# Kernel tuning notes

Measured on AMD Instinct MI355X. Metric: run time of the kernel, lower is better.

## Reference

```python
import jax, jax.numpy as jnp
import numpy as np

E = 8            # num_experts
DIM = 2880       # model dim
HID = 2880       # expert hidden dim (mlp1 outputs 2*HID, interleaved glu/linear)
T = 16384        # total dispatched tokens, evenly split across experts
SWIGLU_LIMIT = 7.0
ALPHA = 1.702


def swiglu(x, alpha=ALPHA, limit=SWIGLU_LIMIT):
    # interleaved: even channels -> glu gate, odd channels -> linear
    x_glu = x[..., ::2]
    x_lin = x[..., 1::2]
    x_glu = jnp.minimum(x_glu, limit)
    x_lin = jnp.clip(x_lin, -limit, limit)
    return x_glu * jax.nn.sigmoid(alpha * x_glu) * (x_lin + 1.0)


def setup_inputs() -> dict:
    key = jax.random.key(0)
    k1, k2, k3, k4, k5 = jax.random.split(key, 5)
    scale = 0.02
    x = jax.random.normal(k1, (T, DIM), dtype=jnp.float32)
    num_tokens_per_expert = jnp.full((E,), T // E, dtype=jnp.int64)
    mlp1_weight = jax.random.normal(k2, (E, 2 * HID, DIM), dtype=jnp.float32) * scale
    mlp1_bias = jax.random.normal(k3, (E, 2 * HID), dtype=jnp.float32) * scale
    mlp2_weight = jax.random.normal(k4, (E, DIM, HID), dtype=jnp.float32) * scale
    mlp2_bias = jax.random.normal(k5, (E, DIM), dtype=jnp.float32) * scale
    return {
        "x": x,
        "num_tokens_per_expert": num_tokens_per_expert,
        "mlp1_weight": mlp1_weight,
        "mlp1_bias": mlp1_bias,
        "mlp2_weight": mlp2_weight,
        "mlp2_bias": mlp2_bias,
    }


def reference(x, num_tokens_per_expert, mlp1_weight, mlp1_bias, mlp2_weight, mlp2_bias):
    # Equal token counts per expert (as constructed): grouped GEMM == batched GEMM
    # over a reshaped [E, T/E, DIM] view. tp_degree == 1 so ScaleBiasForward is identity.
    tpe = T // E
    xg = x.reshape(E, tpe, DIM)                                  # [E, t, D]
    h = jnp.einsum("etd,ehd->eth", xg, mlp1_weight)              # [E, t, 2H]
    h = h + mlp1_bias[:, None, :]
    h = swiglu(h)                                                # [E, t, H]
    out = jnp.einsum("eth,edh->etd", h, mlp2_weight)             # [E, t, D]
    out = out + mlp2_bias[:, None, :]
    return out.reshape(T, DIM)
```

## Files before the change

### kernel.cpp

```cpp
#include <hip/hip_runtime.h>
#include <hip/hip_bf16.h>


#define TT   16384
#define DIM_ 2880
#define HID_ 2880
#define NE   8
#define TPE  2048
#define KDIM 2880

typedef __attribute__((ext_vector_type(8))) short short8;
typedef __attribute__((ext_vector_type(4))) float f32x4;

__device__ __forceinline__ unsigned short f2bf(float f) {
  unsigned u = __builtin_bit_cast(unsigned, f);
  u += 0x7fffu + ((u >> 16) & 1u);
  return (unsigned short)(u >> 16);
}

__global__ void __launch_bounds__(256) cvt_f32_bf16(const float* __restrict__ src,
                                                    unsigned short* __restrict__ dst,
                                                    long n) {
  long i = ((long)blockIdx.x * 256 + threadIdx.x) * 8;
  if (i >= n) return;
  float4 a = *(const float4*)(src + i);
  float4 b = *(const float4*)(src + i + 4);
  union { unsigned short u[8]; short8 v; } r;
  r.u[0] = f2bf(a.x); r.u[1] = f2bf(a.y); r.u[2] = f2bf(a.z); r.u[3] = f2bf(a.w);
  r.u[4] = f2bf(b.x); r.u[5] = f2bf(b.y); r.u[6] = f2bf(b.z); r.u[7] = f2bf(b.w);
  *(short8*)(dst + i) = r.v;
}

template<int BN, int FN, bool FUSE_SWIGLU>
__global__ void __launch_bounds__(256) gemm_bt(const unsigned short* __restrict__ A,
                                               const unsigned short* __restrict__ B,
                                               const float* __restrict__ bias,
                                               void* __restrict__ Cout,
                                               int M, int N) {
  constexpr int BM = 128, BK = 64;
  const int tid  = threadIdx.x;
  const int lane = tid & 63;
  const int wid  = tid >> 6;
  const int wr   = wid >> 1, wc = wid & 1;
  const int e    = blockIdx.z;
  const int m0   = blockIdx.y * BM;
  const int n0   = blockIdx.x * BN;

  __shared__ unsigned short As[BM * BK];
  __shared__ unsigned short Bs[BN * BK];

  const unsigned short* Ae = A + (size_t)e * M * KDIM + (size_t)m0 * KDIM;
  const unsigned short* Be = B + (size_t)e * N * KDIM + (size_t)n0 * KDIM;

  f32x4 acc[4][FN] = {};

  const int srow = tid >> 3;
  const int scol = (tid & 7) * 8;

  for (int kt = 0; kt < KDIM / BK; ++kt) {
    const unsigned short* ak = Ae + kt * BK + scol;
    const unsigned short* bk = Be + kt * BK + scol;
#pragma unroll
    for (int j = 0; j < BM / 32; ++j)
      __builtin_amdgcn_global_load_lds(
          (const __attribute__((address_space(1))) unsigned int*)(ak + (size_t)(j * 32 + srow) * KDIM),
          (__attribute__((address_space(3))) unsigned int*)(&As[j * 2048 + tid * 8]),
          16, 0, 0);
#pragma unroll
    for (int j = 0; j < BN / 32; ++j)
      __builtin_amdgcn_global_load_lds(
          (const __attribute__((address_space(1))) unsigned int*)(bk + (size_t)(j * 32 + srow) * KDIM),
          (__attribute__((address_space(3))) unsigned int*)(&Bs[j * 2048 + tid * 8]),
          16, 0, 0);
    __syncthreads();

#pragma unroll
    for (int ks = 0; ks < 2; ++ks) {
      short8 af[4];
#pragma unroll
      for (int fm = 0; fm < 4; ++fm)
        af[fm] = *(const short8*)&As[(wr * 64 + fm * 16 + (lane & 15)) * BK + ks * 32 + (lane >> 4) * 8];
#pragma unroll
      for (int fn = 0; fn < FN; ++fn) {
        short8 bf = *(const short8*)&Bs[(wc * (FN * 16) + fn * 16 + (lane & 15)) * BK + ks * 32 + (lane >> 4) * 8];
#pragma unroll
        for (int fm = 0; fm < 4; ++fm)
          acc[fm][fn] = __builtin_amdgcn_mfma_f32_16x16x32_bf16(af[fm], bf, acc[fm][fn], 0, 0, 0);
      }
    }
    __syncthreads();
  }

  const float* be = bias + (size_t)e * N;
  if constexpr (FUSE_SWIGLU) {
    unsigned short* ha = (unsigned short*)Cout + (size_t)e * M * (N / 2);
#pragma unroll
    for (int fm = 0; fm < 4; ++fm)
#pragma unroll
      for (int fn = 0; fn < FN; ++fn) {
        const int col = n0 + wc * (FN * 16) + fn * 16 + (lane & 15);
        const float bc = be[col];
#pragma unroll
        for (int j = 0; j < 4; ++j) {
          const int row = m0 + wr * 64 + fm * 16 + (lane >> 4) * 4 + j;
          float v = acc[fm][fn][j] + bc;
          float p = __shfl_xor(v, 1);
          if (!(lane & 1)) {
            float g  = fminf(v, 7.0f);
            float l2 = fminf(fmaxf(p, -7.0f), 7.0f);
            float act = g / (1.0f + __expf(-1.702f * g)) * (l2 + 1.0f);
            ha[(size_t)row * (N / 2) + (col >> 1)] = f2bf(act);
          }
        }
      }
  } else {
    float* out = (float*)Cout + (size_t)e * M * N;
#pragma unroll
    for (int fm = 0; fm < 4; ++fm)
#pragma unroll
      for (int fn = 0; fn < FN; ++fn) {
        const int col = n0 + wc * (FN * 16) + fn * 16 + (lane & 15);
        const float bc = be[col];
#pragma unroll
        for (int j = 0; j < 4; ++j) {
          const int row = m0 + wr * 64 + fm * 16 + (lane >> 4) * 4 + j;
          out[(size_t)row * N + col] = acc[fm][fn][j] + bc;
        }
      }
  }
}

extern "C" void kernel_launch(void* const* d_in, const int* in_sizes, int n_in,
                              void* d_out, int out_size, void* d_ws, size_t ws_size,
                              hipStream_t stream) {
  const float* x  = (const float*)d_in[0];
  const float* w1 = (const float*)d_in[2];
  const float* b1 = (const float*)d_in[3];
  const float* w2 = (const float*)d_in[4];
  const float* b2 = (const float*)d_in[5];

  unsigned short* xb  = (unsigned short*)d_ws;
  unsigned short* w1b = xb  + (size_t)TT * DIM_;
  unsigned short* w2b = w1b + (size_t)NE * 2 * HID_ * DIM_;
  unsigned short* ha  = w2b + (size_t)NE * DIM_ * HID_;

  const long nx = (long)TT * DIM_;
  const long n1 = (long)NE * 2 * HID_ * DIM_;
  const long n2 = (long)NE * DIM_ * HID_;
  cvt_f32_bf16<<<(int)(nx / 2048), 256, 0, stream>>>(x,  xb,  nx);
  cvt_f32_bf16<<<(int)(n1 / 2048), 256, 0, stream>>>(w1, w1b, n1);
  cvt_f32_bf16<<<(int)(n2 / 2048), 256, 0, stream>>>(w2, w2b, n2);

  dim3 g1(2 * HID_ / 128, TPE / 128, NE);
  gemm_bt<128, 4, true><<<g1, 256, 0, stream>>>(xb, w1b, b1, ha, TPE, 2 * HID_);

  dim3 g2(DIM_ / 96, TPE / 128, NE);
  gemm_bt<96, 3, false><<<g2, 256, 0, stream>>>(ha, w2b, b2, (float*)d_out, TPE, DIM_);
}
```

Measured before the change: 1.388 ms.

## Replace GEMMs with 8-wave 256x192 double-buffered pipelined kernel with LDS swizzle

Replaces the single-buffered 128xBN GEMM with a 512-thread kernel using 256x192 tiles. Global-to-LDS loads are double-buffered with explicit vmcnt waits so the next K tile streams in while MFMAs run. The LDS layout is XOR-swizzled to avoid bank conflicts, and block indices are remapped to group tiles for better L2 reuse. The larger tile raises register pressure and shrinks the grid, which could hurt occupancy or leave a tail wave.

```diff
diff --git a/kernel.cpp b/kernel.cpp
--- a/kernel.cpp
+++ b/kernel.cpp
@@ -8,6 +8,7 @@
 #define NE   8
 #define TPE  2048
 #define KDIM 2880
+#define NT   45
 
 typedef __attribute__((ext_vector_type(8))) short short8;
 typedef __attribute__((ext_vector_type(4))) float f32x4;
@@ -31,99 +32,141 @@
   *(short8*)(dst + i) = r.v;
 }
 
-template<int BN, int FN, bool FUSE_SWIGLU>
-__global__ void __launch_bounds__(256) gemm_bt(const unsigned short* __restrict__ A,
-                                               const unsigned short* __restrict__ B,
-                                               const float* __restrict__ bias,
-                                               void* __restrict__ Cout,
-                                               int M, int N) {
-  constexpr int BM = 128, BK = 64;
+template<bool FUSE_SWIGLU>
+__global__ void __launch_bounds__(512, 2) gemm8(const unsigned short* __restrict__ A,
+                                                const unsigned short* __restrict__ B,
+                                                const float* __restrict__ bias,
+                                                void* __restrict__ Cout,
+                                                int M, int N) {
+  __shared__ unsigned short As[2][256 * 64];
+  __shared__ unsigned short Bs[2][192 * 64];
+
   const int tid  = threadIdx.x;
   const int lane = tid & 63;
   const int wid  = tid >> 6;
-  const int wr   = wid >> 1, wc = wid & 1;
+  const int wr   = wid >> 2;
+  const int wc   = wid & 3;
   const int e    = blockIdx.z;
-  const int m0   = blockIdx.y * BM;
-  const int n0   = blockIdx.x * BN;
-
-  __shared__ unsigned short As[BM * BK];
-  __shared__ unsigned short Bs[BN * BK];
-
-  const unsigned short* Ae = A + (size_t)e * M * KDIM + (size_t)m0 * KDIM;
-  const unsigned short* Be = B + (size_t)e * N * KDIM + (size_t)n0 * KDIM;
-
-  f32x4 acc[4][FN] = {};
+
+  const int ntn   = N / 192;
+  const int ntm   = M / 256;
+  const int per_e = ntn * ntm;
+  const int bid   = blockIdx.x;
+  const int swz   = (bid & 7) * (per_e >> 3) + (bid >> 3);
+  const int m0    = (swz / ntn) * 256;
+  const int n0    = (swz % ntn) * 192;
 
   const int srow = tid >> 3;
-  const int scol = (tid & 7) * 8;
-
-  for (int kt = 0; kt < KDIM / BK; ++kt) {
-    const unsigned short* ak = Ae + kt * BK + scol;
-    const unsigned short* bk = Be + kt * BK + scol;
-#pragma unroll
-    for (int j = 0; j < BM / 32; ++j)
+  const int scol = (((tid & 7) ^ (srow & 7)) << 4) >> 1;
+  const unsigned short* Aexp = A + ((size_t)e * M + m0 + srow) * KDIM + scol;
+  const unsigned short* Bexp = B + ((size_t)e * N + n0 + srow) * KDIM + scol;
+
+  auto stage = [&](int buf, int kt) {
+    const unsigned short* asrc = Aexp + (size_t)kt * 64;
+#pragma unroll
+    for (int j = 0; j < 4; ++j)
       __builtin_amdgcn_global_load_lds(
-          (const __attribute__((address_space(1))) unsigned int*)(ak + (size_t)(j * 32 + srow) * KDIM),
-          (__attribute__((address_space(3))) unsigned int*)(&As[j * 2048 + tid * 8]),
+          (const __attribute__((address_space(1))) unsigned int*)(asrc + (size_t)(j * 64) * KDIM),
+          (__attribute__((address_space(3))) unsigned int*)(&As[buf][j * 4096 + tid * 8]),
           16, 0, 0);
-#pragma unroll
-    for (int j = 0; j < BN / 32; ++j)
+    const unsigned short* bsrc = Bexp + (size_t)kt * 64;
+#pragma unroll
+    for (int j = 0; j < 3; ++j)
       __builtin_amdgcn_global_load_lds(
-          (const __attribute__((address_space(1))) unsigned int*)(bk + (size_t)(j * 32 + srow) * KDIM),
-          (__attribute__((address_space(3))) unsigned int*)(&Bs[j * 2048 + tid * 8]),
+          (const __attribute__((address_space(1))) unsigned int*)(bsrc + (size_t)(j * 64) * KDIM),
+          (__attribute__((address_space(3))) unsigned int*)(&Bs[buf][j * 4096 + tid * 8]),
           16, 0, 0);
-    __syncthreads();
-
-#pragma unroll
-    for (int ks = 0; ks < 2; ++ks) {
-      short8 af[4];
-#pragma unroll
-      for (int fm = 0; fm < 4; ++fm)
-        af[fm] = *(const short8*)&As[(wr * 64 + fm * 16 + (lane & 15)) * BK + ks * 32 + (lane >> 4) * 8];
-#pragma unroll
-      for (int fn = 0; fn < FN; ++fn) {
-        short8 bf = *(const short8*)&Bs[(wc * (FN * 16) + fn * 16 + (lane & 15)) * BK + ks * 32 + (lane >> 4) * 8];
-#pragma unroll
-        for (int fm = 0; fm < 4; ++fm)
-          acc[fm][fn] = __builtin_amdgcn_mfma_f32_16x16x32_bf16(af[fm], bf, acc[fm][fn], 0, 0, 0);
-      }
+  };
+
+  const int arow_off = (wr * 128 + (lane & 15)) * 128;
+  const int brow_off = (wc * 48  + (lane & 15)) * 128;
+  const int swzb = (lane & 7) << 4;
+  const int kb   = ((lane >> 4) & 3) * 16;
+  const int c0 = kb ^ swzb;
+  const int c1 = (64 + kb) ^ swzb;
+
+  f32x4 acc[8][3] = {};
+
+  stage(0, 0);
+  stage(1, 1);
+  asm volatile("s_waitcnt vmcnt(7)" ::: "memory");
+  __builtin_amdgcn_s_barrier();
+
+  for (int t = 0; t < NT; ++t) {
+    const int cur = t & 1;
+    const char* aB = (const char*)(&As[cur][0]) + arow_off;
+    const char* bB = (const char*)(&Bs[cur][0]) + brow_off;
+
+    short8 a0[8], a1[8], b0[3], b1[3];
+#pragma unroll
+    for (int fm = 0; fm < 8; ++fm) {
+      a0[fm] = *(const short8*)(aB + fm * 2048 + c0);
+      a1[fm] = *(const short8*)(aB + fm * 2048 + c1);
     }
-    __syncthreads();
+#pragma unroll
+    for (int fn = 0; fn < 3; ++fn) {
+      b0[fn] = *(const short8*)(bB + fn * 2048 + c0);
+      b1[fn] = *(const short8*)(bB + fn * 2048 + c1);
+    }
+
+#pragma unroll
+    for (int fn = 0; fn < 3; ++fn)
+#pragma unroll
+      for (int fm = 0; fm < 8; ++fm)
+        acc[fm][fn] = __builtin_amdgcn_mfma_f32_16x16x32_bf16(a0[fm], b0[fn], acc[fm][fn], 0, 0, 0);
+
+    asm volatile("s_waitcnt lgkmcnt(0)" ::: "memory");
+    __builtin_amdgcn_s_barrier();
+
+    const bool more = (t + 2 < NT);
+    if (more) stage(cur, t + 2);
+
+    __builtin_amdgcn_s_setprio(1);
+#pragma unroll
+    for (int fn = 0; fn < 3; ++fn)
+#pragma unroll
+      for (int fm = 0; fm < 8; ++fm)
+        acc[fm][fn] = __builtin_amdgcn_mfma_f32_16x16x32_bf16(a1[fm], b1[fn], acc[fm][fn], 0, 0, 0);
+    __builtin_amdgcn_s_setprio(0);
+
+    if (more) asm volatile("s_waitcnt vmcnt(7)" ::: "memory");
+    else      asm volatile("s_waitcnt vmcnt(0)" ::: "memory");
+    __builtin_amdgcn_s_barrier();
   }
 
   const float* be = bias + (size_t)e * N;
   if constexpr (FUSE_SWIGLU) {
-    unsigned short* ha = (unsigned short*)Cout + (size_t)e * M * (N / 2);
-#pragma unroll
-    for (int fm = 0; fm < 4; ++fm)
-#pragma unroll
-      for (int fn = 0; fn < FN; ++fn) {
-        const int col = n0 + wc * (FN * 16) + fn * 16 + (lane & 15);
+    unsigned short* ha = (unsigned short*)Cout + (size_t)e * M * (N >> 1);
+#pragma unroll
+    for (int fm = 0; fm < 8; ++fm)
+#pragma unroll
+      for (int fn = 0; fn < 3; ++fn) {
+        const int col = n0 + wc * 48 + fn * 16 + (lane & 15);
         const float bc = be[col];
 #pragma unroll
         for (int j = 0; j < 4; ++j) {
-          const int row = m0 + wr * 64 + fm * 16 + (lane >> 4) * 4 + j;
+          const int row = m0 + wr * 128 + fm * 16 + (lane >> 4) * 4 + j;
           float v = acc[fm][fn][j] + bc;
           float p = __shfl_xor(v, 1);
           if (!(lane & 1)) {
             float g  = fminf(v, 7.0f);
             float l2 = fminf(fmaxf(p, -7.0f), 7.0f);
             float act = g / (1.0f + __expf(-1.702f * g)) * (l2 + 1.0f);
-            ha[(size_t)row * (N / 2) + (col >> 1)] = f2bf(act);
+            ha[(size_t)row * (N >> 1) + (col >> 1)] = f2bf(act);
           }
         }
       }
   } else {
     float* out = (float*)Cout + (size_t)e * M * N;
 #pragma unroll
-    for (int fm = 0; fm < 4; ++fm)
-#pragma unroll
-      for (int fn = 0; fn < FN; ++fn) {
-        const int col = n0 + wc * (FN * 16) + fn * 16 + (lane & 15);
+    for (int fm = 0; fm < 8; ++fm)
+#pragma unroll
+      for (int fn = 0; fn < 3; ++fn) {
+        const int col = n0 + wc * 48 + fn * 16 + (lane & 15);
         const float bc = be[col];
 #pragma unroll
         for (int j = 0; j < 4; ++j) {
-          const int row = m0 + wr * 64 + fm * 16 + (lane >> 4) * 4 + j;
+          const int row = m0 + wr * 128 + fm * 16 + (lane >> 4) * 4 + j;
           out[(size_t)row * N + col] = acc[fm][fn][j] + bc;
         }
       }
@@ -151,9 +194,9 @@
   cvt_f32_bf16<<<(int)(n1 / 2048), 256, 0, stream>>>(w1, w1b, n1);
   cvt_f32_bf16<<<(int)(n2 / 2048), 256, 0, stream>>>(w2, w2b, n2);
 
-  dim3 g1(2 * HID_ / 128, TPE / 128, NE);
-  gemm_bt<128, 4, true><<<g1, 256, 0, stream>>>(xb, w1b, b1, ha, TPE, 2 * HID_);
-
-  dim3 g2(DIM_ / 96, TPE / 128, NE);
-  gemm_bt<96, 3, false><<<g2, 256, 0, stream>>>(ha, w2b, b2, (float*)d_out, TPE, DIM_);
-}
+  dim3 g1((5760 / 192) * (TPE / 256), 1, NE);
+  gemm8<true><<<g1, 512, 0, stream>>>(xb, w1b, b1, ha, TPE, 5760);
+
+  dim3 g2((DIM_ / 192) * (TPE / 256), 1, NE);
+  gemm8<false><<<g2, 512, 0, stream>>>(ha, w2b, b2, (float*)d_out, TPE, DIM_);
+}
```

New measurement: 1.252 ms. -9.8%, faster.
